# Kernel optimization log

Hardware: AMD Instinct MI355X
Metric: run time of the kernel (lower is better)

## Reference

```python
import jax, jax.numpy as jnp
import numpy as np

Q, M, D = 4096, 100000, 1536

def _l2norm(x, eps=1e-12):
    return x / jnp.maximum(jnp.linalg.norm(x, axis=1, keepdims=True), eps)

def setup_inputs() -> dict:
    key = jax.random.key(0)
    kq, km = jax.random.split(key)
    # patch features are L2-normalized in _extract_patches (F.normalize p=2)
    query = _l2norm(jax.random.normal(kq, (Q, D), dtype=jnp.float32))
    memory = _l2norm(jax.random.normal(km, (M, D), dtype=jnp.float32))
    return {"query": query, "memory": memory}

def reference(query, memory):
    # torch.cdist(query, memory) (p=2) followed by min over memory dim.
    # dist^2 = |q|^2 + |m|^2 - 2 q.m  -> sqrt, clamped at 0 for numerics.
    q2 = jnp.sum(query * query, axis=1, keepdims=True)          # [Q, 1]
    m2 = jnp.sum(memory * memory, axis=1)                        # [M]
    d2 = q2 + m2[None, :] - 2.0 * (query @ memory.T)             # [Q, M]
    dists = jnp.sqrt(jnp.maximum(d2, 0.0))
    nn_dists = jnp.min(dists, axis=1)                            # [Q]
    anomaly_score = jnp.max(nn_dists)                            # scalar, predict()'s score
    return nn_dists, anomaly_score
```

## Files before the change

### kernel.cpp

```cpp
#include <hip/hip_runtime.h>
#include <hip/hip_bf16.h>
#include <float.h>


#define QN 4096
#define MN 100000
#define MP 100096
#define DN 1536
#define NT 24
#define BK 32
#define NKIT (DN / BK)

typedef __attribute__((ext_vector_type(8))) short short8;
typedef __attribute__((ext_vector_type(4))) float float4v;
typedef __attribute__((ext_vector_type(4))) short short4v;
typedef __attribute__((address_space(1))) const unsigned g_u32;
typedef __attribute__((address_space(3))) unsigned l_u32;

__device__ __forceinline__ short f2bf(float f) {
    unsigned u = __float_as_uint(f);
    u += 0x7FFFu + ((u >> 16) & 1u);
    return (short)(u >> 16);
}
__device__ __forceinline__ unsigned encf(float f) {
    unsigned u = __float_as_uint(f);
    return (u & 0x80000000u) ? ~u : (u | 0x80000000u);
}
__device__ __forceinline__ float decf(unsigned e) {
    unsigned u = (e & 0x80000000u) ? (e & 0x7FFFFFFFu) : ~e;
    return __uint_as_float(u);
}
__device__ __forceinline__ void gload_lds16(const void* g, void* l) {
    __builtin_amdgcn_global_load_lds((g_u32*)g, (l_u32*)l, 16, 0, 0);
}

__global__ void init_min(unsigned* __restrict__ dminEnc) {
    int i = blockIdx.x * blockDim.x + threadIdx.x;
    if (i < QN) dminEnc[i] = 0xFF7FFFFFu;
}

__global__ void cvt_bf16(const float* __restrict__ src, short* __restrict__ dst,
                         long n_valid, long n_total) {
    long i = ((long)blockIdx.x * blockDim.x + threadIdx.x) * 4;
    if (i >= n_total) return;
    if (i + 4 <= n_valid) {
        float4 v = *(const float4*)(src + i);
        short4v o = { f2bf(v.x), f2bf(v.y), f2bf(v.z), f2bf(v.w) };
        *(short4v*)(dst + i) = o;
    } else {
        for (int j = 0; j < 4; ++j)
            if (i + j < n_total) dst[i + j] = (i + j < n_valid) ? f2bf(src[i + j]) : 0;
    }
}

#define SUB_OFF(b, h, R, C) ((((((b) * 2 + (h)) * 8 + (R)) * 2) + (C)) * 512)

__global__ __launch_bounds__(512, 2)
void nn_gemm_bf16_256(const short* __restrict__ qB, const short* __restrict__ mB,
                      unsigned* __restrict__ dminEnc)
{
    __shared__ short A_lds[2 * 2 * 8 * 2 * 512];
    __shared__ short B_lds[2 * 2 * 8 * 2 * 512];

    const int tid = threadIdx.x;
    const int l   = tid & 63;
    const int w   = tid >> 6;
    const int wm  = w >> 2;
    const int wn  = w & 3;
    const int l15 = l & 15;
    const int q4  = l >> 4;

    const int qb = blockIdx.x * 256;
    const int mb = blockIdx.y * 256;

    const int rlane = l >> 2;
    const int csw   = ((l & 3) ^ ((l >> 5) << 1)) * 8;
    const int sh    = w >> 2;
    const int saR   = w & 3;
    const int sbR   = ((w >> 1) & 1) * 4 + (w & 1);

    const short* pAlo = qB + (size_t)(qb + sh * 128 + saR * 16 + rlane) * DN + csw;
    const short* pAhi = pAlo + (size_t)64 * DN;
    const short* pBc0 = mB + (size_t)(mb + sh * 128 + sbR * 16 + rlane) * DN + csw;
    const short* pBc1 = pBc0 + (size_t)32 * DN;

    const int inoff = l15 * 64 + ((q4 ^ (((l >> 3) & 1) << 1))) * 16;
    const char* aP = (const char*)A_lds + wm * 16384 + inoff;
    const char* bP = (const char*)B_lds + (wn >> 1) * 16384 + (wn & 1) * 8192 + inoff;

    short8 af[4][2], bf[2][2];
    float4v acc[8][4];
#pragma unroll
    for (int fi = 0; fi < 8; ++fi)
#pragma unroll
        for (int cj = 0; cj < 4; ++cj)
            acc[fi][cj] = (float4v){0.f, 0.f, 0.f, 0.f};

#define STAGE_ALO(b, ko) do { \
        gload_lds16(pAlo + (ko),      &A_lds[SUB_OFF(b, sh, saR,     0)]); \
        gload_lds16(pAlo + (ko) + 32, &A_lds[SUB_OFF(b, sh, saR,     1)]); } while (0)
#define STAGE_AHI(b, ko) do { \
        gload_lds16(pAhi + (ko),      &A_lds[SUB_OFF(b, sh, saR + 4, 0)]); \
        gload_lds16(pAhi + (ko) + 32, &A_lds[SUB_OFF(b, sh, saR + 4, 1)]); } while (0)
#define STAGE_BC0(b, ko) do { \
        gload_lds16(pBc0 + (ko),      &B_lds[SUB_OFF(b, sh, sbR,     0)]); \
        gload_lds16(pBc0 + (ko) + 32, &B_lds[SUB_OFF(b, sh, sbR,     1)]); } while (0)
#define STAGE_BC1(b, ko) do { \
        gload_lds16(pBc1 + (ko),      &B_lds[SUB_OFF(b, sh, sbR + 2, 0)]); \
        gload_lds16(pBc1 + (ko) + 32, &B_lds[SUB_OFF(b, sh, sbR + 2, 1)]); } while (0)

#define LDA(b, RH) do { _Pragma("unroll") \
        for (int m_ = 0; m_ < 4; ++m_) { \
            af[m_][0] = *(const short8*)(aP + (b) * 32768 + ((RH) * 4 + m_) * 2048); \
            af[m_][1] = *(const short8*)(aP + (b) * 32768 + ((RH) * 4 + m_) * 2048 + 1024); } } while (0)
#define LDB(b, CH) do { _Pragma("unroll") \
        for (int n_ = 0; n_ < 2; ++n_) { \
            bf[n_][0] = *(const short8*)(bP + (b) * 32768 + ((CH) * 2 + n_) * 2048); \
            bf[n_][1] = *(const short8*)(bP + (b) * 32768 + ((CH) * 2 + n_) * 2048 + 1024); } } while (0)

#define MMA(RH, CH) do { _Pragma("unroll") \
        for (int m_ = 0; m_ < 4; ++m_) { _Pragma("unroll") \
            for (int n_ = 0; n_ < 2; ++n_) { \
                acc[(RH) * 4 + m_][(CH) * 2 + n_] = __builtin_amdgcn_mfma_f32_16x16x32_bf16( \
                    af[m_][0], bf[n_][0], acc[(RH) * 4 + m_][(CH) * 2 + n_], 0, 0, 0); \
                acc[(RH) * 4 + m_][(CH) * 2 + n_] = __builtin_amdgcn_mfma_f32_16x16x32_bf16( \
                    af[m_][1], bf[n_][1], acc[(RH) * 4 + m_][(CH) * 2 + n_], 0, 0, 0); } } } while (0)

#define MID(RH, CH) \
        __builtin_amdgcn_s_barrier(); \
        __builtin_amdgcn_s_setprio(1); \
        MMA(RH, CH); \
        __builtin_amdgcn_s_setprio(0);
#define TAIL \
        __builtin_amdgcn_s_barrier();
#define TAIL_VM6 \
        asm volatile("s_waitcnt vmcnt(6)" ::: "memory"); \
        __builtin_amdgcn_s_barrier();
#define TAIL_VM0 \
        asm volatile("s_waitcnt vmcnt(0)" ::: "memory"); \
        __builtin_amdgcn_s_barrier();

    STAGE_ALO(0, 0); STAGE_AHI(0, 0); STAGE_BC0(0, 0); STAGE_BC1(0, 0);
    STAGE_ALO(1, 64); STAGE_BC1(1, 64); STAGE_AHI(1, 64);
    asm volatile("s_waitcnt vmcnt(6)" ::: "memory");
    __builtin_amdgcn_s_barrier();

    for (int it = 0; it < NT / 2 - 1; ++it) {
        const int kT1 = (it * 2 + 1) * 64;
        const int kT2 = kT1 + 64;
        const int kT3 = kT1 + 128;
        STAGE_BC0(1, kT1); LDB(0, 0); LDA(0, 0);
        MID(0, 0) TAIL
        STAGE_ALO(0, kT2); LDB(0, 1);
        MID(0, 1) TAIL
        STAGE_BC1(0, kT2); LDA(0, 1);
        MID(1, 1) TAIL
        STAGE_AHI(0, kT2); LDB(0, 0);
        MID(1, 0) TAIL_VM6
        STAGE_BC0(0, kT2); LDB(1, 0); LDA(1, 0);
        MID(0, 0) TAIL
        STAGE_ALO(1, kT3); LDB(1, 1);
        MID(0, 1) TAIL
        STAGE_BC1(1, kT3); LDA(1, 1);
        MID(1, 1) TAIL
        STAGE_AHI(1, kT3); LDB(1, 0);
        MID(1, 0) TAIL_VM6
    }
    STAGE_BC0(1, (NT - 1) * 64); LDB(0, 0); LDA(0, 0);
    MID(0, 0) TAIL
    LDB(0, 1);
    MID(0, 1) TAIL
    LDA(0, 1);
    MID(1, 1) TAIL
    LDB(0, 0);
    MID(1, 0) TAIL_VM0
    LDB(1, 0); LDA(1, 0);
    MID(0, 0) TAIL
    LDB(1, 1);
    MID(0, 1) TAIL
    LDA(1, 1);
    MID(1, 1) TAIL
    LDB(1, 0);
    MID(1, 0)

#undef STAGE_ALO
#undef STAGE_AHI
#undef STAGE_BC0
#undef STAGE_BC1
#undef LDA
#undef LDB
#undef MMA
#undef MID
#undef TAIL
#undef TAIL_VM6
#undef TAIL_VM0

    unsigned* qmin = (unsigned*)A_lds;
    __syncthreads();
    if (tid < 256) qmin[tid] = 0xFFFFFFFFu;
    __syncthreads();

#pragma unroll
    for (int fi = 0; fi < 8; ++fi) {
#pragma unroll
        for (int r = 0; r < 4; ++r) {
            float v = FLT_MAX;
#pragma unroll
            for (int cj = 0; cj < 4; ++cj) {
                const int gcol = mb + wn * 64 + cj * 16 + l15;
                const float d2 = fmaf(-2.0f, acc[fi][cj][r], 2.0f);
                v = fminf(v, (gcol < MN) ? d2 : FLT_MAX);
            }
            v = fminf(v, __shfl_xor(v, 1));
            v = fminf(v, __shfl_xor(v, 2));
            v = fminf(v, __shfl_xor(v, 4));
            v = fminf(v, __shfl_xor(v, 8));
            if (l15 == 0)
                atomicMin(&qmin[wm * 128 + fi * 16 + q4 * 4 + r], encf(v));
        }
    }
    __syncthreads();
    if (tid < 256) atomicMin(&dminEnc[qb + tid], qmin[tid]);
}

#define LDSS 40
__global__ __launch_bounds__(256, 2)
void nn_gemm_f32(const float* __restrict__ query, const float* __restrict__ memory,
                 unsigned* __restrict__ dminEnc)
{
    __shared__ __align__(16) short As[128 * LDSS];
    __shared__ __align__(16) short Bs[128 * LDSS];
    __shared__ unsigned qmin[128];

    const int tid = threadIdx.x, lane = tid & 63, wave = tid >> 6;
    const int wrow = wave >> 1, wcol = wave & 1, quad = lane >> 4, l16 = lane & 15;
    const int qb = blockIdx.x * 128, mb = blockIdx.y * 128;
    if (tid < 128) qmin[tid] = 0xFFFFFFFFu;

    int rowS[4], c4S[4];
    const float *aPtr[4], *bPtr[4];
    bool bValid[4];
#pragma unroll
    for (int s = 0; s < 4; ++s) {
        int idx = s * 256 + tid, row = idx >> 3, c4 = idx & 7;
        rowS[s] = row; c4S[s] = c4;
        aPtr[s] = query + (size_t)(qb + row) * DN + c4 * 4;
        int gr = mb + row;
        bValid[s] = (gr < MN);
        bPtr[s] = memory + (size_t)(bValid[s] ? gr : 0) * DN + c4 * 4;
    }
    float4 aReg[4], bReg[4];
#pragma unroll
    for (int s = 0; s < 4; ++s) {
        aReg[s] = *(const float4*)(aPtr[s]);
        bReg[s] = bValid[s] ? *(const float4*)(bPtr[s]) : make_float4(0.f, 0.f, 0.f, 0.f);
    }
    float4v acc[4][4];
#pragma unroll
    for (int mi = 0; mi < 4; ++mi)
#pragma unroll
        for (int ni = 0; ni < 4; ++ni) acc[mi][ni] = (float4v){0.f, 0.f, 0.f, 0.f};

    for (int kk = 0; kk < NKIT; ++kk) {
#pragma unroll
        for (int s = 0; s < 4; ++s) {
            short4v pa = { f2bf(aReg[s].x), f2bf(aReg[s].y), f2bf(aReg[s].z), f2bf(aReg[s].w) };
            short4v pb = { f2bf(bReg[s].x), f2bf(bReg[s].y), f2bf(bReg[s].z), f2bf(bReg[s].w) };
            *(short4v*)&As[rowS[s] * LDSS + c4S[s] * 4] = pa;
            *(short4v*)&Bs[rowS[s] * LDSS + c4S[s] * 4] = pb;
        }
        __syncthreads();
        if (kk + 1 < NKIT) {
            const int ko = (kk + 1) * BK;
#pragma unroll
            for (int s = 0; s < 4; ++s) {
                aReg[s] = *(const float4*)(aPtr[s] + ko);
                bReg[s] = bValid[s] ? *(const float4*)(bPtr[s] + ko)
                                    : make_float4(0.f, 0.f, 0.f, 0.f);
            }
        }
        short8 af[4], bfr[4];
#pragma unroll
        for (int mi = 0; mi < 4; ++mi)
            af[mi] = *(const short8*)&As[(wrow * 64 + mi * 16 + l16) * LDSS + quad * 8];
#pragma unroll
        for (int ni = 0; ni < 4; ++ni)
            bfr[ni] = *(const short8*)&Bs[(wcol * 64 + ni * 16 + l16) * LDSS + quad * 8];
#pragma unroll
        for (int mi = 0; mi < 4; ++mi)
#pragma unroll
            for (int ni = 0; ni < 4; ++ni)
                acc[mi][ni] = __builtin_amdgcn_mfma_f32_16x16x32_bf16(
                    af[mi], bfr[ni], acc[mi][ni], 0, 0, 0);
        __syncthreads();
    }
#pragma unroll
    for (int mi = 0; mi < 4; ++mi) {
#pragma unroll
        for (int r = 0; r < 4; ++r) {
            float v = FLT_MAX;
#pragma unroll
            for (int ni = 0; ni < 4; ++ni) {
                int gcol = mb + wcol * 64 + ni * 16 + l16;
                float d2 = fmaf(-2.0f, acc[mi][ni][r], 2.0f);
                v = fminf(v, (gcol < MN) ? d2 : FLT_MAX);
            }
            v = fminf(v, __shfl_xor(v, 1));
            v = fminf(v, __shfl_xor(v, 2));
            v = fminf(v, __shfl_xor(v, 4));
            v = fminf(v, __shfl_xor(v, 8));
            if (l16 == 0)
                atomicMin(&qmin[wrow * 64 + mi * 16 + quad * 4 + r], encf(v));
        }
    }
    __syncthreads();
    if (tid < 128) atomicMin(&dminEnc[qb + tid], qmin[tid]);
}

__global__ void finalize(const unsigned* __restrict__ dminEnc, float* __restrict__ out) {
    __shared__ float red[256];
    const int tid = threadIdx.x;
    float mx = 0.f;
    for (int i = tid; i < QN; i += 256) {
        float d2 = decf(dminEnc[i]);
        float d = sqrtf(fmaxf(d2, 0.f));
        out[i] = d;
        mx = fmaxf(mx, d);
    }
    red[tid] = mx;
    __syncthreads();
    for (int s = 128; s > 0; s >>= 1) {
        if (tid < s) red[tid] = fmaxf(red[tid], red[tid + s]);
        __syncthreads();
    }
    if (tid == 0) out[QN] = red[0];
}

extern "C" void kernel_launch(void* const* d_in, const int* in_sizes, int n_in,
                              void* d_out, int out_size, void* d_ws, size_t ws_size,
                              hipStream_t stream)
{
    const float* query  = (const float*)d_in[0];
    const float* memory = (const float*)d_in[1];
    float* out = (float*)d_out;

    const size_t memB_elems = (size_t)MP * DN;
    const size_t qB_elems   = (size_t)QN * DN;
    const size_t need = memB_elems * 2 + qB_elems * 2 + (size_t)QN * 4;

    if (ws_size >= need) {
        short* mB = (short*)d_ws;
        short* qB = mB + memB_elems;
        unsigned* dminEnc = (unsigned*)(qB + qB_elems);

        hipLaunchKernelGGL(init_min, dim3((QN + 255) / 256), dim3(256), 0, stream, dminEnc);
        {
            long nv = (long)MN * DN, nt = (long)memB_elems;
            int blocks = (int)((nt / 4 + 255) / 256);
            hipLaunchKernelGGL(cvt_bf16, dim3(blocks), dim3(256), 0, stream,
                               memory, mB, nv, nt);
        }
        {
            long nv = (long)qB_elems, nt = (long)qB_elems;
            int blocks = (int)((nt / 4 + 255) / 256);
            hipLaunchKernelGGL(cvt_bf16, dim3(blocks), dim3(256), 0, stream,
                               query, qB, nv, nt);
        }
        hipLaunchKernelGGL(nn_gemm_bf16_256, dim3(QN / 256, MP / 256), dim3(512), 0, stream,
                           qB, mB, dminEnc);
        hipLaunchKernelGGL(finalize, dim3(1), dim3(256), 0, stream, dminEnc, out);
    } else {
        unsigned* dminEnc = (unsigned*)d_ws;
        hipLaunchKernelGGL(init_min, dim3((QN + 255) / 256), dim3(256), 0, stream, dminEnc);
        hipLaunchKernelGGL(nn_gemm_f32, dim3(QN / 128, (MN + 127) / 128), dim3(256), 0, stream,
                           query, memory, dminEnc);
        hipLaunchKernelGGL(finalize, dim3(1), dim3(256), 0, stream, dminEnc, out);
    }
}
```

Before: 2.485 ms.

## Software-pipeline LDS fragment reads with MFMA using double-buffered B registers

Restructures the main GEMM loop so LDS reads of the next A and B fragments are interleaved with the MFMA groups of the current sub-tile, using a double-buffered B fragment register set. Before, each phase did its LDS loads, then a barrier, then MFMAs. Now loads are issued ahead and overlap with matrix math, and the vmcnt wait thresholds are adjusted to match. This costs more VGPRs for the extra B buffer, which could lower occupancy or cause spills, and the hand-ordered barriers and waits must stay correct.

```diff
diff --git a/kernel.cpp b/kernel.cpp
--- a/kernel.cpp
+++ b/kernel.cpp
@@ -88,7 +88,8 @@
     const char* aP = (const char*)A_lds + wm * 16384 + inoff;
     const char* bP = (const char*)B_lds + (wn >> 1) * 16384 + (wn & 1) * 8192 + inoff;
 
-    short8 af[4][2], bf[2][2];
+    short8 af[4][2];
+    short8 bf[2][2][2];
     float4v acc[8][4];
 #pragma unroll
     for (int fi = 0; fi < 8; ++fi)
@@ -109,91 +110,129 @@
         gload_lds16(pBc1 + (ko),      &B_lds[SUB_OFF(b, sh, sbR + 2, 0)]); \
         gload_lds16(pBc1 + (ko) + 32, &B_lds[SUB_OFF(b, sh, sbR + 2, 1)]); } while (0)
 
-#define LDA(b, RH) do { _Pragma("unroll") \
-        for (int m_ = 0; m_ < 4; ++m_) { \
-            af[m_][0] = *(const short8*)(aP + (b) * 32768 + ((RH) * 4 + m_) * 2048); \
-            af[m_][1] = *(const short8*)(aP + (b) * 32768 + ((RH) * 4 + m_) * 2048 + 1024); } } while (0)
-#define LDB(b, CH) do { _Pragma("unroll") \
+#define RD_B(S, b, CH) do { _Pragma("unroll") \
         for (int n_ = 0; n_ < 2; ++n_) { \
-            bf[n_][0] = *(const short8*)(bP + (b) * 32768 + ((CH) * 2 + n_) * 2048); \
-            bf[n_][1] = *(const short8*)(bP + (b) * 32768 + ((CH) * 2 + n_) * 2048 + 1024); } } while (0)
-
-#define MMA(RH, CH) do { _Pragma("unroll") \
-        for (int m_ = 0; m_ < 4; ++m_) { _Pragma("unroll") \
-            for (int n_ = 0; n_ < 2; ++n_) { \
-                acc[(RH) * 4 + m_][(CH) * 2 + n_] = __builtin_amdgcn_mfma_f32_16x16x32_bf16( \
-                    af[m_][0], bf[n_][0], acc[(RH) * 4 + m_][(CH) * 2 + n_], 0, 0, 0); \
-                acc[(RH) * 4 + m_][(CH) * 2 + n_] = __builtin_amdgcn_mfma_f32_16x16x32_bf16( \
-                    af[m_][1], bf[n_][1], acc[(RH) * 4 + m_][(CH) * 2 + n_], 0, 0, 0); } } } while (0)
-
-#define MID(RH, CH) \
-        __builtin_amdgcn_s_barrier(); \
-        __builtin_amdgcn_s_setprio(1); \
-        MMA(RH, CH); \
-        __builtin_amdgcn_s_setprio(0);
-#define TAIL \
-        __builtin_amdgcn_s_barrier();
-#define TAIL_VM6 \
-        asm volatile("s_waitcnt vmcnt(6)" ::: "memory"); \
-        __builtin_amdgcn_s_barrier();
-#define TAIL_VM0 \
-        asm volatile("s_waitcnt vmcnt(0)" ::: "memory"); \
-        __builtin_amdgcn_s_barrier();
+            bf[S][n_][0] = *(const short8*)(bP + (b) * 32768 + ((CH) * 2 + n_) * 2048); \
+            bf[S][n_][1] = *(const short8*)(bP + (b) * 32768 + ((CH) * 2 + n_) * 2048 + 1024); } } while (0)
+#define RD_A1(b, RH, m) do { \
+        af[m][0] = *(const short8*)(aP + (b) * 32768 + ((RH) * 4 + (m)) * 2048); \
+        af[m][1] = *(const short8*)(aP + (b) * 32768 + ((RH) * 4 + (m)) * 2048 + 1024); } while (0)
+
+#define MMA_G(S, RH, CH, m) do { _Pragma("unroll") \
+        for (int n_ = 0; n_ < 2; ++n_) { \
+            acc[(RH) * 4 + (m)][(CH) * 2 + n_] = __builtin_amdgcn_mfma_f32_16x16x32_bf16( \
+                af[m][0], bf[S][n_][0], acc[(RH) * 4 + (m)][(CH) * 2 + n_], 0, 0, 0); \
+            acc[(RH) * 4 + (m)][(CH) * 2 + n_] = __builtin_amdgcn_mfma_f32_16x16x32_bf16( \
+                af[m][1], bf[S][n_][1], acc[(RH) * 4 + (m)][(CH) * 2 + n_], 0, 0, 0); } } while (0)
+
+#define BAR   __builtin_amdgcn_s_barrier()
+#define PRIO1 __builtin_amdgcn_s_setprio(1)
+#define PRIO0 __builtin_amdgcn_s_setprio(0)
+#define VM4   asm volatile("s_waitcnt vmcnt(4)" ::: "memory")
+#define VM6   asm volatile("s_waitcnt vmcnt(6)" ::: "memory")
+#define VM0   asm volatile("s_waitcnt vmcnt(0)" ::: "memory")
 
     STAGE_ALO(0, 0); STAGE_AHI(0, 0); STAGE_BC0(0, 0); STAGE_BC1(0, 0);
     STAGE_ALO(1, 64); STAGE_BC1(1, 64); STAGE_AHI(1, 64);
-    asm volatile("s_waitcnt vmcnt(6)" ::: "memory");
-    __builtin_amdgcn_s_barrier();
+    VM6;
+    BAR;
+    RD_B(0, 0, 0);
+    RD_A1(0, 0, 0); RD_A1(0, 0, 1); RD_A1(0, 0, 2); RD_A1(0, 0, 3);
 
     for (int it = 0; it < NT / 2 - 1; ++it) {
         const int kT1 = (it * 2 + 1) * 64;
         const int kT2 = kT1 + 64;
         const int kT3 = kT1 + 128;
-        STAGE_BC0(1, kT1); LDB(0, 0); LDA(0, 0);
-        MID(0, 0) TAIL
-        STAGE_ALO(0, kT2); LDB(0, 1);
-        MID(0, 1) TAIL
-        STAGE_BC1(0, kT2); LDA(0, 1);
-        MID(1, 1) TAIL
-        STAGE_AHI(0, kT2); LDB(0, 0);
-        MID(1, 0) TAIL_VM6
-        STAGE_BC0(0, kT2); LDB(1, 0); LDA(1, 0);
-        MID(0, 0) TAIL
-        STAGE_ALO(1, kT3); LDB(1, 1);
-        MID(0, 1) TAIL
-        STAGE_BC1(1, kT3); LDA(1, 1);
-        MID(1, 1) TAIL
-        STAGE_AHI(1, kT3); LDB(1, 0);
-        MID(1, 0) TAIL_VM6
-    }
-    STAGE_BC0(1, (NT - 1) * 64); LDB(0, 0); LDA(0, 0);
-    MID(0, 0) TAIL
-    LDB(0, 1);
-    MID(0, 1) TAIL
-    LDA(0, 1);
-    MID(1, 1) TAIL
-    LDB(0, 0);
-    MID(1, 0) TAIL_VM0
-    LDB(1, 0); LDA(1, 0);
-    MID(0, 0) TAIL
-    LDB(1, 1);
-    MID(0, 1) TAIL
-    LDA(1, 1);
-    MID(1, 1) TAIL
-    LDB(1, 0);
-    MID(1, 0)
+        RD_B(1, 0, 1); STAGE_BC0(1, kT1);
+        PRIO1; MMA_G(0,0,0,0); MMA_G(0,0,0,1); MMA_G(0,0,0,2); MMA_G(0,0,0,3); PRIO0;
+        BAR;
+        PRIO1;
+        MMA_G(1,0,1,0); RD_A1(0,1,0);
+        MMA_G(1,0,1,1); RD_A1(0,1,1);
+        MMA_G(1,0,1,2); RD_A1(0,1,2);
+        MMA_G(1,0,1,3); RD_A1(0,1,3);
+        PRIO0; STAGE_ALO(0, kT2);
+        BAR;
+        RD_B(0, 0, 0); STAGE_BC1(0, kT2);
+        PRIO1; MMA_G(1,1,1,0); MMA_G(1,1,1,1); MMA_G(1,1,1,2); MMA_G(1,1,1,3); PRIO0;
+        VM4;
+        BAR;
+        RD_B(1, 1, 0); STAGE_AHI(0, kT2);
+        PRIO1;
+        MMA_G(0,1,0,0); RD_A1(1,0,0);
+        MMA_G(0,1,0,1); RD_A1(1,0,1);
+        MMA_G(0,1,0,2); RD_A1(1,0,2);
+        MMA_G(0,1,0,3); RD_A1(1,0,3);
+        PRIO0; BAR;
+        RD_B(0, 1, 1); STAGE_BC0(0, kT2);
+        PRIO1; MMA_G(1,0,0,0); MMA_G(1,0,0,1); MMA_G(1,0,0,2); MMA_G(1,0,0,3); PRIO0;
+        BAR;
+        STAGE_ALO(1, kT3);
+        PRIO1;
+        MMA_G(0,0,1,0); RD_A1(1,1,0);
+        MMA_G(0,0,1,1); RD_A1(1,1,1);
+        MMA_G(0,0,1,2); RD_A1(1,1,2);
+        MMA_G(0,0,1,3); RD_A1(1,1,3);
+        PRIO0; BAR;
+        RD_B(1, 1, 0); STAGE_BC1(1, kT3);
+        PRIO1; MMA_G(0,1,1,0); MMA_G(0,1,1,1); MMA_G(0,1,1,2); MMA_G(0,1,1,3); PRIO0;
+        VM4;
+        BAR;
+        RD_B(0, 0, 0); STAGE_AHI(1, kT3);
+        PRIO1;
+        MMA_G(1,1,0,0); RD_A1(0,0,0);
+        MMA_G(1,1,0,1); RD_A1(0,0,1);
+        MMA_G(1,1,0,2); RD_A1(0,0,2);
+        MMA_G(1,1,0,3); RD_A1(0,0,3);
+        PRIO0; BAR;
+    }
+    RD_B(1, 0, 1); STAGE_BC0(1, (NT - 1) * 64);
+    PRIO1; MMA_G(0,0,0,0); MMA_G(0,0,0,1); MMA_G(0,0,0,2); MMA_G(0,0,0,3); PRIO0;
+    BAR;
+    PRIO1;
+    MMA_G(1,0,1,0); RD_A1(0,1,0);
+    MMA_G(1,0,1,1); RD_A1(0,1,1);
+    MMA_G(1,0,1,2); RD_A1(0,1,2);
+    MMA_G(1,0,1,3); RD_A1(0,1,3);
+    PRIO0; BAR;
+    RD_B(0, 0, 0);
+    PRIO1; MMA_G(1,1,1,0); MMA_G(1,1,1,1); MMA_G(1,1,1,2); MMA_G(1,1,1,3); PRIO0;
+    VM0;
+    BAR;
+    RD_B(1, 1, 0);
+    PRIO1;
+    MMA_G(0,1,0,0); RD_A1(1,0,0);
+    MMA_G(0,1,0,1); RD_A1(1,0,1);
+    MMA_G(0,1,0,2); RD_A1(1,0,2);
+    MMA_G(0,1,0,3); RD_A1(1,0,3);
+    PRIO0; BAR;
+    RD_B(0, 1, 1);
+    PRIO1; MMA_G(1,0,0,0); MMA_G(1,0,0,1); MMA_G(1,0,0,2); MMA_G(1,0,0,3); PRIO0;
+    BAR;
+    PRIO1;
+    MMA_G(0,0,1,0); RD_A1(1,1,0);
+    MMA_G(0,0,1,1); RD_A1(1,1,1);
+    MMA_G(0,0,1,2); RD_A1(1,1,2);
+    MMA_G(0,0,1,3); RD_A1(1,1,3);
+    PRIO0; BAR;
+    RD_B(1, 1, 0);
+    PRIO1; MMA_G(0,1,1,0); MMA_G(0,1,1,1); MMA_G(0,1,1,2); MMA_G(0,1,1,3); PRIO0;
+    BAR;
+    PRIO1; MMA_G(1,1,0,0); MMA_G(1,1,0,1); MMA_G(1,1,0,2); MMA_G(1,1,0,3); PRIO0;
 
 #undef STAGE_ALO
 #undef STAGE_AHI
 #undef STAGE_BC0
 #undef STAGE_BC1
-#undef LDA
-#undef LDB
-#undef MMA
-#undef MID
-#undef TAIL
-#undef TAIL_VM6
-#undef TAIL_VM0
+#undef RD_B
+#undef RD_A1
+#undef MMA_G
+#undef BAR
+#undef PRIO1
+#undef PRIO0
+#undef VM4
+#undef VM6
+#undef VM0
 
     unsigned* qmin = (unsigned*)A_lds;
     __syncthreads();
```

New measurement: 2.121 ms. -14.7%, faster.
